# Performance work log

Measured on AMD Instinct MI355X. Metric: run time of the kernel, lower is better.

The kernel has to match this reference:

```python
import jax, jax.numpy as jnp
import numpy as np

B, G, T, F_IN = 32, 128, 128, 318


def _lin(x, W, b):
    # torch Linear: y = x @ W.T + b, W: (out, in)
    return x @ W.T + b


def _sap(rep, W1, b1, W2, b2):
    # SelfAttentionPooling over second-to-last axis. rep: (..., T, H)
    s = _lin(jax.nn.relu(_lin(rep, W1, b1)), W2, b2)[..., 0]  # (..., T)
    w = jax.nn.softmax(s, axis=-1)
    return jnp.einsum('...th,...t->...h', rep, w)  # (..., H)


def setup_inputs() -> dict:
    key = jax.random.key(0)
    ks = jax.random.split(key, 20)

    def w(k, shape, fan_in):
        bound = 1.0 / np.sqrt(fan_in)
        return jax.random.uniform(k, shape, jnp.float32, -bound, bound)

    inp = {
        'x': jax.random.normal(ks[0], (B, G, T, F_IN), jnp.float32),
        # model1: 318->50->20->20
        'W1a': w(ks[1], (50, 318), 318), 'b1a': w(ks[2], (50,), 318),
        'W1b': w(ks[3], (20, 50), 50),  'b1b': w(ks[4], (20,), 50),
        'W1c': w(ks[5], (20, 20), 20),  'b1c': w(ks[6], (20,), 20),
        # model2 pooling (input_dim=20, hidden=10)
        'pW1': w(ks[7], (10, 20), 20),  'pb1': w(ks[8], (10,), 20),
        'pW2': w(ks[9], (1, 10), 10),   'pb2': w(ks[10], (1,), 10),
        # model2_1 pooling
        'qW1': w(ks[11], (10, 20), 20), 'qb1': w(ks[12], (10,), 20),
        'qW2': w(ks[13], (1, 10), 10),  'qb2': w(ks[14], (1,), 10),
        # model3: 20->10->1
        'W3a': w(ks[15], (10, 20), 20), 'b3a': w(ks[16], (10,), 20),
        'W3b': w(ks[17], (1, 10), 10),  'b3b': w(ks[18], (1,), 10),
    }
    return inp


def reference(x, W1a, b1a, W1b, b1b, W1c, b1c, pW1, pb1, pW2, pb2,
              qW1, qb1, qW2, qb2, W3a, b3a, W3b, b3b):
    # model1 MLP on features: (B,G,T,318) -> (B,G,T,20)
    h = jax.nn.relu(_lin(x, W1a, b1a))
    h = jax.nn.relu(_lin(h, W1b, b1b))
    h = jax.nn.relu(_lin(h, W1c, b1c))
    # pool over T: (B,G,20)
    r = _sap(h, pW1, pb1, pW2, pb2)
    # pool over G: (B,20)
    r = _sap(r, qW1, qb1, qW2, qb2)
    # F.normalize (L2 over dim=1, eps=1e-12)
    norm = jnp.linalg.norm(r, axis=-1, keepdims=True)
    r = r / jnp.maximum(norm, 1e-12)
    # model3: (B,1)
    out = _lin(jax.nn.relu(_lin(r, W3a, b3a)), W3b, b3b)
    return out
```

## Files before the change

### kernel.cpp

```cpp
#include <hip/hip_runtime.h>
#include <hip/hip_bf16.h>
#include <math.h>
#include <stdint.h>

typedef __attribute__((ext_vector_type(8))) short bf16x8;
typedef __attribute__((ext_vector_type(4))) float floatx4;

static __device__ __forceinline__ unsigned short f32_to_bf16_rne(float f) {
    union { float f; uint32_t u; } v; v.f = f;
    uint32_t u = v.u;
    return (unsigned short)((u + 0x7fffu + ((u >> 16) & 1u)) >> 16);
}
static __device__ __forceinline__ float bf16_to_f32(unsigned short h) {
    union { uint32_t u; float f; } v; v.u = ((uint32_t)h) << 16;
    return v.f;
}
static __device__ __forceinline__ bf16x8 cvt8(float4 a, float4 b) {
    union { __hip_bfloat162 h[4]; bf16x8 v; } u;
    u.h[0] = __float22bfloat162_rn({a.x, a.y});
    u.h[1] = __float22bfloat162_rn({a.z, a.w});
    u.h[2] = __float22bfloat162_rn({b.x, b.y});
    u.h[3] = __float22bfloat162_rn({b.z, b.w});
    return u.v;
}

#define BAR() do { \
    asm volatile("s_waitcnt lgkmcnt(0)" ::: "memory"); \
    __builtin_amdgcn_s_barrier(); \
    asm volatile("" ::: "memory"); } while (0)

__global__ void prep_w(const float* __restrict__ W1a, unsigned short* __restrict__ Bpre) {
    int idx = blockIdx.x * 256 + threadIdx.x;
    if (idx >= 40960) return;
    int e  = idx & 7;
    int n  = (idx >> 3) & 63;
    int kq = (idx >> 9) & 3;
    int p  = (idx >> 11) & 1;
    int ks = idx >> 12;
    int k  = ks * 32 + kq * 8 + e;
    float w = (n < 50 && k < 318) ? W1a[n * 318 + k] : 0.0f;
    unsigned short hi = f32_to_bf16_rne(w);
    Bpre[idx] = (p == 0) ? hi : f32_to_bf16_rne(w - bf16_to_f32(hi));
}

#define SLAB (64 * 318)
#define H1W 52

__global__ __launch_bounds__(256, 3)
void gemm_h1(const float* __restrict__ x,
             const unsigned short* __restrict__ Bpre,
             const float* __restrict__ b1a,
             uint32_t* __restrict__ h1b)
{
    __shared__ __align__(16) char bsm[40960];

    const int tid  = threadIdx.x;
    const int wv   = tid >> 6;
    const int lane = tid & 63;
    const int fr   = lane & 15;
    const int kq   = lane >> 4;

    const float* arow = x + (size_t)blockIdx.x * SLAB + (wv * 16 + fr) * 318 + kq * 8;

    floatx4 gb[10];
    #pragma unroll
    for (int j = 0; j < 10; ++j)
        gb[j] = *(const floatx4*)((const char*)Bpre + (j * 256 + tid) * 16);

    float4 af[20];
    #pragma unroll
    for (int ks = 0; ks < 10; ++ks)
        #pragma unroll
        for (int j = 0; j < 2; ++j) {
            if (ks == 9 && kq == 3 && j == 1) {
                float2 t = *(const float2*)(arow + 9 * 32 + 4);
                af[19] = make_float4(t.x, t.y, 0.f, 0.f);
            } else {
                af[ks * 2 + j] = *(const float4*)(arow + ks * 32 + 4 * j);
            }
        }
    __builtin_amdgcn_sched_barrier(0);

    #pragma unroll
    for (int j = 0; j < 10; ++j)
        *(floatx4*)(bsm + (j * 256 + tid) * 16) = gb[j];
    #pragma unroll
    for (int j = 0; j < 10; ++j)
        gb[j] = *(const floatx4*)((const char*)Bpre + 40960 + (j * 256 + tid) * 16);
    __builtin_amdgcn_sched_barrier(0);
    BAR();

    floatx4 acc[4];
    #pragma unroll
    for (int nf = 0; nf < 4; ++nf) acc[nf] = (floatx4){0.f, 0.f, 0.f, 0.f};

    #pragma unroll
    for (int ks = 0; ks < 5; ++ks) {
        const char* bb = bsm + ks * 8192 + (kq << 10) + (fr << 4);
        bf16x8 a = cvt8(af[ks * 2], af[ks * 2 + 1]);
        #pragma unroll
        for (int nf = 0; nf < 4; ++nf) {
            bf16x8 bh = *(const bf16x8*)(bb + nf * 256);
            bf16x8 bl = *(const bf16x8*)(bb + 4096 + nf * 256);
            acc[nf] = __builtin_amdgcn_mfma_f32_16x16x32_bf16(a, bh, acc[nf], 0, 0, 0);
            acc[nf] = __builtin_amdgcn_mfma_f32_16x16x32_bf16(a, bl, acc[nf], 0, 0, 0);
        }
    }
    BAR();

    #pragma unroll
    for (int j = 0; j < 10; ++j)
        *(floatx4*)(bsm + (j * 256 + tid) * 16) = gb[j];
    BAR();

    #pragma unroll
    for (int ks = 5; ks < 10; ++ks) {
        const char* bb = bsm + (ks - 5) * 8192 + (kq << 10) + (fr << 4);
        bf16x8 a = cvt8(af[ks * 2], af[ks * 2 + 1]);
        #pragma unroll
        for (int nf = 0; nf < 4; ++nf) {
            bf16x8 bh = *(const bf16x8*)(bb + nf * 256);
            bf16x8 bl = *(const bf16x8*)(bb + 4096 + nf * 256);
            acc[nf] = __builtin_amdgcn_mfma_f32_16x16x32_bf16(a, bh, acc[nf], 0, 0, 0);
            acc[nf] = __builtin_amdgcn_mfma_f32_16x16x32_bf16(a, bl, acc[nf], 0, 0, 0);
        }
    }

    {
        const size_t tp0 = (size_t)blockIdx.x * 32 + wv * 8 + kq * 2;
        uint32_t* hw = h1b + tp0 * H1W;
        #pragma unroll
        for (int nf = 0; nf < 4; ++nf) {
            int n = nf * 16 + fr;
            if (n < 50) {
                float bia = b1a[n];
                float v0 = fmaxf(acc[nf][0] + bia, 0.0f);
                float v1 = fmaxf(acc[nf][1] + bia, 0.0f);
                float v2 = fmaxf(acc[nf][2] + bia, 0.0f);
                float v3 = fmaxf(acc[nf][3] + bia, 0.0f);
                hw[n]       = (uint32_t)f32_to_bf16_rne(v0) | ((uint32_t)f32_to_bf16_rne(v1) << 16);
                hw[H1W + n] = (uint32_t)f32_to_bf16_rne(v2) | ((uint32_t)f32_to_bf16_rne(v3) << 16);
            }
        }
    }
}

__global__ __launch_bounds__(256, 4)
void tail_pool(const uint32_t* __restrict__ h1b,
               const float* __restrict__ W1b, const float* __restrict__ b1b,
               const float* __restrict__ W1c, const float* __restrict__ b1c,
               const float* __restrict__ pW1, const float* __restrict__ pb1,
               const float* __restrict__ pW2, const float* __restrict__ pb2,
               float* __restrict__ partials)
{
    const int t    = blockIdx.x * 256 + threadIdx.x;
    const int lane = threadIdx.x & 63;
    const int sh   = (t & 1) * 16;

    float hv[50];
    {
        const uint2* hr = (const uint2*)(h1b + (size_t)(t >> 1) * H1W);
        #pragma unroll
        for (int j = 0; j < 25; ++j) {
            uint2 u = hr[j];
            hv[2 * j]     = bf16_to_f32((unsigned short)(u.x >> sh));
            hv[2 * j + 1] = bf16_to_f32((unsigned short)(u.y >> sh));
        }
    }

    float h2[20];
    #pragma unroll
    for (int o = 0; o < 20; ++o) h2[o] = b1b[o];
    #pragma unroll
    for (int i = 0; i < 50; ++i) {
        float hvv = hv[i];
        #pragma unroll
        for (int o = 0; o < 20; ++o) h2[o] = fmaf(hvv, W1b[o * 50 + i], h2[o]);
    }
    #pragma unroll
    for (int o = 0; o < 20; ++o) h2[o] = fmaxf(h2[o], 0.0f);

    float h3[20];
    #pragma unroll
    for (int o = 0; o < 20; ++o) {
        float a = b1c[o];
        const float* w = W1c + o * 20;
        #pragma unroll
        for (int i = 0; i < 20; ++i) a = fmaf(h2[i], w[i], a);
        h3[o] = fmaxf(a, 0.0f);
    }

    float s = pb2[0];
    #pragma unroll
    for (int j = 0; j < 10; ++j) {
        float a = pb1[j];
        const float* w = pW1 + j * 20;
        #pragma unroll
        for (int i = 0; i < 20; ++i) a = fmaf(h3[i], w[i], a);
        s = fmaf(fmaxf(a, 0.0f), pW2[j], s);
    }

    float m = s;
    #pragma unroll
    for (int d = 32; d > 0; d >>= 1) m = fmaxf(m, __shfl_xor(m, d));
    float e = expf(s - m);
    float S = e;
    #pragma unroll
    for (int d = 32; d > 0; d >>= 1) S += __shfl_xor(S, d);

    float V[20];
    #pragma unroll
    for (int o = 0; o < 20; ++o) {
        float v = e * h3[o];
        #pragma unroll
        for (int d = 32; d > 0; d >>= 1) v += __shfl_xor(v, d);
        V[o] = v;
    }

    float myv = m;
    if (lane == 1) myv = S;
    #pragma unroll
    for (int o = 0; o < 20; ++o) if (lane == o + 2) myv = V[o];
    if (lane < 22) partials[(size_t)(t >> 6) * 24 + lane] = myv;
}

__global__ __launch_bounds__(128, 4)
void pool_g_head(const float* __restrict__ partials,
                 const float* __restrict__ qW1, const float* __restrict__ qb1,
                 const float* __restrict__ qW2, const float* __restrict__ qb2,
                 const float* __restrict__ W3a, const float* __restrict__ b3a,
                 const float* __restrict__ W3b, const float* __restrict__ b3b,
                 float* __restrict__ out)
{
    __shared__ float red_m[2];
    __shared__ float red_s[2];
    __shared__ float part[2][20];

    const int tid = threadIdx.x;
    const int b = blockIdx.x;
    const float* P = partials + ((size_t)(b * 128 + tid)) * 48;

    float m0 = P[0], S0 = P[1], m1 = P[24], S1 = P[25];
    float m = fmaxf(m0, m1);
    float w0 = expf(m0 - m), w1 = expf(m1 - m);
    float den = fmaf(S0, w0, S1 * w1);

    float v[20];
    #pragma unroll
    for (int o = 0; o < 20; ++o)
        v[o] = fmaf(P[2 + o], w0, P[26 + o] * w1) / den;

    float s = qb2[0];
    #pragma unroll
    for (int j = 0; j < 10; ++j) {
        float a = qb1[j];
        const float* w = qW1 + j * 20;
        #pragma unroll
        for (int i = 0; i < 20; ++i) a = fmaf(v[i], w[i], a);
        s = fmaf(fmaxf(a, 0.0f), qW2[j], s);
    }

    const int wig = tid >> 6, lane = tid & 63;
    float mm = s;
    #pragma unroll
    for (int d = 32; d > 0; d >>= 1) mm = fmaxf(mm, __shfl_xor(mm, d));
    if (lane == 0) red_m[wig] = mm;
    __syncthreads();
    mm = fmaxf(red_m[0], red_m[1]);

    float e = expf(s - mm);
    float su = e;
    #pragma unroll
    for (int d = 32; d > 0; d >>= 1) su += __shfl_xor(su, d);
    if (lane == 0) red_s[wig] = su;

    #pragma unroll
    for (int o = 0; o < 20; ++o) {
        float val = e * v[o];
        #pragma unroll
        for (int d = 32; d > 0; d >>= 1) val += __shfl_xor(val, d);
        if (lane == 0) part[wig][o] = val;
    }
    __syncthreads();

    if (tid == 0) {
        float dg = red_s[0] + red_s[1];
        float rb[20];
        float n2 = 0.0f;
        #pragma unroll
        for (int o = 0; o < 20; ++o) {
            rb[o] = (part[0][o] + part[1][o]) / dg;
            n2 = fmaf(rb[o], rb[o], n2);
        }
        float nrm = fmaxf(sqrtf(n2), 1e-12f);
        #pragma unroll
        for (int o = 0; o < 20; ++o) rb[o] /= nrm;

        float accv = b3b[0];
        #pragma unroll
        for (int j = 0; j < 10; ++j) {
            float a = b3a[j];
            const float* w = W3a + j * 20;
            #pragma unroll
            for (int i = 0; i < 20; ++i) a = fmaf(rb[i], w[i], a);
            accv = fmaf(fmaxf(a, 0.0f), W3b[j], accv);
        }
        out[b] = accv;
    }
}

extern "C" void kernel_launch(void* const* d_in, const int* in_sizes, int n_in,
                              void* d_out, int out_size, void* d_ws, size_t ws_size,
                              hipStream_t stream) {
    const float* x   = (const float*)d_in[0];
    const float* W1a = (const float*)d_in[1];
    const float* b1a = (const float*)d_in[2];
    const float* W1b = (const float*)d_in[3];
    const float* b1b = (const float*)d_in[4];
    const float* W1c = (const float*)d_in[5];
    const float* b1c = (const float*)d_in[6];
    const float* pW1 = (const float*)d_in[7];
    const float* pb1 = (const float*)d_in[8];
    const float* pW2 = (const float*)d_in[9];
    const float* pb2 = (const float*)d_in[10];
    const float* qW1 = (const float*)d_in[11];
    const float* qb1 = (const float*)d_in[12];
    const float* qW2 = (const float*)d_in[13];
    const float* qb2 = (const float*)d_in[14];
    const float* W3a = (const float*)d_in[15];
    const float* b3a = (const float*)d_in[16];
    const float* W3b = (const float*)d_in[17];
    const float* b3b = (const float*)d_in[18];

    float* partials      = (float*)d_ws;
    unsigned short* Bpre = (unsigned short*)((char*)d_ws + 786432);
    uint32_t* h1b        = (uint32_t*)((char*)d_ws + 868352);

    prep_w<<<160, 256, 0, stream>>>(W1a, Bpre);
    gemm_h1<<<8192, 256, 0, stream>>>(x, Bpre, b1a, h1b);
    tail_pool<<<2048, 256, 0, stream>>>(
        h1b, W1b, b1b, W1c, b1c, pW1, pb1, pW2, pb2, partials);
    pool_g_head<<<32, 128, 0, stream>>>(
        partials, qW1, qb1, qW2, qb2, W3a, b3a, W3b, b3b, (float*)d_out);
}
```

Measured before the change: 223.8 us.

## Load B weights directly into LDS via global_load_lds and raise occupancy

Replaces the register-staged copy of the pre-split bf16 W1a tiles (global→VGPR→LDS) with global_load_lds direct-to-LDS transfers, synchronized through vmcnt waits and barriers. This frees the 40 VGPRs that held the gb staging buffers, so launch bounds are raised from 3 to 4 waves-per-EU. The first-half wait uses vmcnt(20) and assumes ordering of the B loads relative to the A loads. The second-half load now sits fully on the critical path between the two MFMA phases instead of being prefetched into registers.

```diff
diff --git a/kernel.cpp b/kernel.cpp
--- a/kernel.cpp
+++ b/kernel.cpp
@@ -24,10 +24,9 @@
     return u.v;
 }
 
-#define BAR() do { \
-    asm volatile("s_waitcnt lgkmcnt(0)" ::: "memory"); \
-    __builtin_amdgcn_s_barrier(); \
-    asm volatile("" ::: "memory"); } while (0)
+#define GLL(g, l) __builtin_amdgcn_global_load_lds( \
+    (const __attribute__((address_space(1))) void*)(g), \
+    (__attribute__((address_space(3))) void*)(l), 16, 0, 0)
 
 __global__ void prep_w(const float* __restrict__ W1a, unsigned short* __restrict__ Bpre) {
     int idx = blockIdx.x * 256 + threadIdx.x;
@@ -46,13 +45,13 @@
 #define SLAB (64 * 318)
 #define H1W 52
 
-__global__ __launch_bounds__(256, 3)
+__global__ __launch_bounds__(256, 4)
 void gemm_h1(const float* __restrict__ x,
              const unsigned short* __restrict__ Bpre,
              const float* __restrict__ b1a,
              uint32_t* __restrict__ h1b)
 {
-    __shared__ __align__(16) char bsm[40960];
+    __shared__ __align__(1024) char bsm[40960];
 
     const int tid  = threadIdx.x;
     const int wv   = tid >> 6;
@@ -62,10 +61,10 @@
 
     const float* arow = x + (size_t)blockIdx.x * SLAB + (wv * 16 + fr) * 318 + kq * 8;
 
-    floatx4 gb[10];
     #pragma unroll
     for (int j = 0; j < 10; ++j)
-        gb[j] = *(const floatx4*)((const char*)Bpre + (j * 256 + tid) * 16);
+        GLL((const char*)Bpre + j * 4096 + wv * 1024 + lane * 16,
+            bsm + j * 4096 + wv * 1024);
 
     float4 af[20];
     #pragma unroll
@@ -81,14 +80,9 @@
         }
     __builtin_amdgcn_sched_barrier(0);
 
-    #pragma unroll
-    for (int j = 0; j < 10; ++j)
-        *(floatx4*)(bsm + (j * 256 + tid) * 16) = gb[j];
-    #pragma unroll
-    for (int j = 0; j < 10; ++j)
-        gb[j] = *(const floatx4*)((const char*)Bpre + 40960 + (j * 256 + tid) * 16);
+    asm volatile("s_waitcnt vmcnt(20)" ::: "memory");
+    __builtin_amdgcn_s_barrier();
     __builtin_amdgcn_sched_barrier(0);
-    BAR();
 
     floatx4 acc[4];
     #pragma unroll
@@ -106,12 +100,17 @@
             acc[nf] = __builtin_amdgcn_mfma_f32_16x16x32_bf16(a, bl, acc[nf], 0, 0, 0);
         }
     }
-    BAR();
+    asm volatile("s_waitcnt lgkmcnt(0)" ::: "memory");
+    __builtin_amdgcn_s_barrier();
+    __builtin_amdgcn_sched_barrier(0);
 
     #pragma unroll
     for (int j = 0; j < 10; ++j)
-        *(floatx4*)(bsm + (j * 256 + tid) * 16) = gb[j];
-    BAR();
+        GLL((const char*)Bpre + 40960 + j * 4096 + wv * 1024 + lane * 16,
+            bsm + j * 4096 + wv * 1024);
+    asm volatile("s_waitcnt vmcnt(0)" ::: "memory");
+    __builtin_amdgcn_s_barrier();
+    __builtin_amdgcn_sched_barrier(0);
 
     #pragma unroll
     for (int ks = 5; ks < 10; ++ks) {
```

Measured after the change: 225.9 us. Within noise of the previous version (+0.9%).
